# Kernel optimization log

Hardware: AMD Instinct MI355X
Metric: run time of the kernel (lower is better)

## Reference

```python
import jax, jax.numpy as jnp
import numpy as np

NUM_BINS = 15
GAMMA_INITIAL = 1.0
EPS = 1e-20


def setup_inputs() -> dict:
    key = jax.random.key(0)
    k1, k2 = jax.random.split(key)
    N, C = 1048576, 128
    inp = jax.random.normal(k1, (N, C), dtype=jnp.float32)
    target = jax.random.randint(k2, (N,), 0, C, dtype=jnp.int64)
    # bin_stats from __init__: bin i covers [i/num_bins, (i+1)/num_bins), gamma=gamma_initial
    bin_uppers = (jnp.arange(1, NUM_BINS, dtype=jnp.float32) / NUM_BINS)  # interior boundaries [num_bins-1]
    gammas = jnp.full((NUM_BINS,), GAMMA_INITIAL, dtype=jnp.float32)
    return {"input": inp, "target": target, "bin_uppers": bin_uppers, "gammas": gammas}


def reference(input, target, bin_uppers, gammas):
    # [N, C] logits -> per-sample logpt at target class
    logp = jax.nn.log_softmax(input, axis=1)                       # [N, C]
    logpt = jnp.take_along_axis(logp, target[:, None], axis=1)[:, 0]  # [N]
    pt = jnp.exp(logpt)                                            # [N]
    # vectorized replacement of the Python bin-search: pt in [lower, upper) -> bin index
    # (first bin catches pt < uppers[0], last bin catches pt >= uppers[-1])
    bin_idx = jnp.searchsorted(bin_uppers, pt, side="right")       # [N] in [0, num_bins-1]
    gamma = gammas[bin_idx]                                        # [N] (gamma lookup, detached in original)
    gamma_sign = jnp.sign(gamma)
    gamma_mag = jnp.abs(gamma)
    loss = -((1.0 - gamma_sign * pt + EPS) ** gamma_mag) * logpt
    return loss.sum()
```

## Files before the change

kernel.cpp:

```cpp
#include <hip/hip_runtime.h>

#define NBINS 15

typedef float f32x4 __attribute__((ext_vector_type(4)));

__device__ __forceinline__ float rdlane_f(float v, int lane) {
    return __int_as_float(__builtin_amdgcn_readlane(__float_as_int(v), lane));
}

template <int CTRL, int RMASK>
__device__ __forceinline__ float dpp_add(float e) {
    int moved = __builtin_amdgcn_update_dpp(0, __float_as_int(e), CTRL, RMASK, 0xf, true);
    return e + __int_as_float(moved);
}

__device__ __forceinline__ float half32_sum(float e) {
    e = dpp_add<0x111, 0xf>(e);
    e = dpp_add<0x112, 0xf>(e);
    e = dpp_add<0x114, 0xf>(e);
    e = dpp_add<0x118, 0xf>(e);
    e = dpp_add<0x142, 0xa>(e);
    return e;
}

__global__ __launch_bounds__(256) void adafocal_partial(
    const float* __restrict__ inp,
    const int* __restrict__ target,
    const float* __restrict__ bin_uppers,
    const float* __restrict__ gammas,
    float* __restrict__ partial,
    int N)
{
    __shared__ float  s_g[NBINS];
    __shared__ float2 s_coll[4][128];
    __shared__ float  s_wsum[4];

    if (threadIdx.x < NBINS) s_g[threadIdx.x] = gammas[threadIdx.x];
    __syncthreads();

    float u[NBINS - 1];
    #pragma unroll
    for (int i = 0; i < NBINS - 1; ++i) u[i] = bin_uppers[i];

    const int lane  = threadIdx.x & 63;
    const int wid   = threadIdx.x >> 6;
    const int gwave = blockIdx.x * 4 + wid;
    const int wrow0 = gwave * 128;

    int2 tt = make_int2(0, 0);
    if (wrow0 + 2 * lane + 1 < N)      tt = ((const int2*)target)[(wrow0 >> 1) + lane];
    else if (wrow0 + 2 * lane < N)     tt.x = target[wrow0 + 2 * lane];

    if (wrow0 + 128 <= N) {
        #pragma unroll 4
        for (int k = 0; k < 64; ++k) {
            const f32x4 v = __builtin_nontemporal_load(
                (const f32x4*)(inp + (size_t)(wrow0 + 2 * k) * 128) + lane);

            float e = __expf(v.x) + __expf(v.y) + __expf(v.z) + __expf(v.w);
            e = half32_sum(e);

            const int t0 = __builtin_amdgcn_readlane(tt.x, k);
            const int t1 = __builtin_amdgcn_readlane(tt.y, k);
            const float a0  = (t0 & 1) ? v.y : v.x;
            const float b0  = (t0 & 1) ? v.w : v.z;
            const float xt0 = rdlane_f((t0 & 2) ? b0 : a0, t0 >> 2);
            const float a1  = (t1 & 1) ? v.y : v.x;
            const float b1  = (t1 & 1) ? v.w : v.z;
            const float xt1 = rdlane_f((t1 & 2) ? b1 : a1, 32 + (t1 >> 2));

            float2 val;
            val.x = e;
            val.y = (lane < 32) ? xt0 : xt1;
            if ((lane & 31) == 31)
                s_coll[wid][2 * k + (lane >> 5)] = val;
        }
    } else {
        s_coll[wid][lane]      = make_float2(1.0f, 0.0f);
        s_coll[wid][64 + lane] = make_float2(1.0f, 0.0f);
        for (int k = 0; k < 64; ++k) {
            const int grow = wrow0 + 2 * k;
            if (grow >= N) break;
            const bool full = (grow + 1 < N);
            f32x4 v = {0.f, 0.f, 0.f, 0.f};
            if (full || lane < 32)
                v = *((const f32x4*)(inp + (size_t)grow * 128) + lane);
            float e = __expf(v.x) + __expf(v.y) + __expf(v.z) + __expf(v.w);
            e = half32_sum(e);
            const int t0 = __builtin_amdgcn_readlane(tt.x, k);
            const int t1 = __builtin_amdgcn_readlane(tt.y, k);
            const float a0  = (t0 & 1) ? v.y : v.x;
            const float b0  = (t0 & 1) ? v.w : v.z;
            const float xt0 = rdlane_f((t0 & 2) ? b0 : a0, t0 >> 2);
            const float a1  = (t1 & 1) ? v.y : v.x;
            const float b1  = (t1 & 1) ? v.w : v.z;
            const float xt1 = rdlane_f((t1 & 2) ? b1 : a1, 32 + (t1 >> 2));
            float2 val;
            val.x = e;
            val.y = (lane < 32) ? xt0 : xt1;
            if (lane == 31 || (full && lane == 63))
                s_coll[wid][2 * k + (lane >> 5)] = val;
        }
    }

    float acc = 0.0f;
    #pragma unroll
    for (int h = 0; h < 2; ++h) {
        const float2 cv   = s_coll[wid][64 * h + lane];
        const float logpt = cv.y - __logf(cv.x);
        const float pt    = __expf(logpt);

        int b = 0;
        #pragma unroll
        for (int i = 0; i < NBINS - 1; ++i)
            b += (u[i] <= pt) ? 1 : 0;

        const float g     = s_g[b];
        const float gsign = (g > 0.0f) ? 1.0f : (g < 0.0f ? -1.0f : 0.0f);
        const float gmag  = fabsf(g);
        const float base  = 1.0f - gsign * pt + 1e-20f;
        const float powv  = (gmag == 1.0f) ? base : __powf(base, gmag);
        acc -= powv * logpt;
    }

    #pragma unroll
    for (int m = 1; m < 64; m <<= 1)
        acc += __shfl_xor(acc, m);
    if (lane == 0) s_wsum[wid] = acc;
    __syncthreads();
    if (threadIdx.x == 0)
        partial[blockIdx.x] = (s_wsum[0] + s_wsum[1]) + (s_wsum[2] + s_wsum[3]);
}

__global__ __launch_bounds__(256) void adafocal_final(
    const float* __restrict__ partial, float* __restrict__ out, int nblocks)
{
    __shared__ float s_wsum[4];
    float acc = 0.0f;
    for (int i = threadIdx.x; i < nblocks; i += 256) acc += partial[i];
    #pragma unroll
    for (int m = 1; m < 64; m <<= 1)
        acc += __shfl_xor(acc, m);
    const int lane = threadIdx.x & 63;
    const int wid  = threadIdx.x >> 6;
    if (lane == 0) s_wsum[wid] = acc;
    __syncthreads();
    if (threadIdx.x == 0)
        out[0] = (s_wsum[0] + s_wsum[1]) + (s_wsum[2] + s_wsum[3]);
}

extern "C" void kernel_launch(void* const* d_in, const int* in_sizes, int n_in,
                              void* d_out, int out_size, void* d_ws, size_t ws_size,
                              hipStream_t stream) {
    const float* inp        = (const float*)d_in[0];
    const int*   targetp    = (const int*)d_in[1];
    const float* bin_uppers = (const float*)d_in[2];
    const float* gammas     = (const float*)d_in[3];
    float* out = (float*)d_out;

    const int N = in_sizes[1];
    const int nwaves  = (N + 127) / 128;
    const int nblocks = (nwaves + 3) / 4;

    float* partial = (float*)d_ws;

    adafocal_partial<<<nblocks, 256, 0, stream>>>(inp, targetp, bin_uppers, gammas, partial, N);
    adafocal_final<<<1, 256, 0, stream>>>(partial, out, nblocks);
}
```

Measured before the change: 95.48 us.

## Fuse final reduction into main kernel via last-block atomic counter

```diff
diff --git a/kernel.cpp b/kernel.cpp
--- a/kernel.cpp
+++ b/kernel.cpp
@@ -6,6 +6,9 @@
 
 __device__ __forceinline__ float rdlane_f(float v, int lane) {
     return __int_as_float(__builtin_amdgcn_readlane(__float_as_int(v), lane));
+}
+__device__ __forceinline__ float rdfirst_f(float v) {
+    return __int_as_float(__builtin_amdgcn_readfirstlane(__float_as_int(v)));
 }
 
 template <int CTRL, int RMASK>
@@ -23,24 +26,27 @@
     return e;
 }
 
-__global__ __launch_bounds__(256) void adafocal_partial(
+__global__ __launch_bounds__(256) void adafocal_fused(
     const float* __restrict__ inp,
     const int* __restrict__ target,
     const float* __restrict__ bin_uppers,
     const float* __restrict__ gammas,
+    float* __restrict__ out,
+    unsigned int* __restrict__ counter,
     float* __restrict__ partial,
     int N)
 {
     __shared__ float  s_g[NBINS];
     __shared__ float2 s_coll[4][128];
     __shared__ float  s_wsum[4];
+    __shared__ int    s_last;
 
     if (threadIdx.x < NBINS) s_g[threadIdx.x] = gammas[threadIdx.x];
     __syncthreads();
 
     float u[NBINS - 1];
     #pragma unroll
-    for (int i = 0; i < NBINS - 1; ++i) u[i] = bin_uppers[i];
+    for (int i = 0; i < NBINS - 1; ++i) u[i] = rdfirst_f(bin_uppers[i]);
 
     const int lane  = threadIdx.x & 63;
     const int wid   = threadIdx.x >> 6;
@@ -52,7 +58,7 @@
     else if (wrow0 + 2 * lane < N)     tt.x = target[wrow0 + 2 * lane];
 
     if (wrow0 + 128 <= N) {
-        #pragma unroll 4
+        #pragma unroll 8
         for (int k = 0; k < 64; ++k) {
             const f32x4 v = __builtin_nontemporal_load(
                 (const f32x4*)(inp + (size_t)(wrow0 + 2 * k) * 128) + lane);
@@ -128,25 +134,29 @@
         acc += __shfl_xor(acc, m);
     if (lane == 0) s_wsum[wid] = acc;
     __syncthreads();
-    if (threadIdx.x == 0)
+
+    if (threadIdx.x == 0) {
         partial[blockIdx.x] = (s_wsum[0] + s_wsum[1]) + (s_wsum[2] + s_wsum[3]);
-}
+        __threadfence();
+        unsigned int old = __hip_atomic_fetch_add(counter, 1u, __ATOMIC_ACQ_REL,
+                                                  __HIP_MEMORY_SCOPE_AGENT);
+        s_last = (old == gridDim.x - 1) ? 1 : 0;
+    }
+    __syncthreads();
 
-__global__ __launch_bounds__(256) void adafocal_final(
-    const float* __restrict__ partial, float* __restrict__ out, int nblocks)
-{
-    __shared__ float s_wsum[4];
-    float acc = 0.0f;
-    for (int i = threadIdx.x; i < nblocks; i += 256) acc += partial[i];
-    #pragma unroll
-    for (int m = 1; m < 64; m <<= 1)
-        acc += __shfl_xor(acc, m);
-    const int lane = threadIdx.x & 63;
-    const int wid  = threadIdx.x >> 6;
-    if (lane == 0) s_wsum[wid] = acc;
-    __syncthreads();
-    if (threadIdx.x == 0)
-        out[0] = (s_wsum[0] + s_wsum[1]) + (s_wsum[2] + s_wsum[3]);
+    if (s_last) {
+        float a2 = 0.0f;
+        for (unsigned int i = threadIdx.x; i < gridDim.x; i += 256)
+            a2 += __hip_atomic_load(&partial[i], __ATOMIC_RELAXED,
+                                    __HIP_MEMORY_SCOPE_AGENT);
+        #pragma unroll
+        for (int m = 1; m < 64; m <<= 1)
+            a2 += __shfl_xor(a2, m);
+        if (lane == 0) s_wsum[wid] = a2;
+        __syncthreads();
+        if (threadIdx.x == 0)
+            out[0] = (s_wsum[0] + s_wsum[1]) + (s_wsum[2] + s_wsum[3]);
+    }
 }
 
 extern "C" void kernel_launch(void* const* d_in, const int* in_sizes, int n_in,
@@ -162,8 +172,10 @@
     const int nwaves  = (N + 127) / 128;
     const int nblocks = (nwaves + 3) / 4;
 
-    float* partial = (float*)d_ws;
+    unsigned int* counter = (unsigned int*)d_ws;
+    float* partial = (float*)((char*)d_ws + 1024);
 
-    adafocal_partial<<<nblocks, 256, 0, stream>>>(inp, targetp, bin_uppers, gammas, partial, N);
-    adafocal_final<<<1, 256, 0, stream>>>(partial, out, nblocks);
+    hipMemsetAsync(counter, 0, sizeof(unsigned int), stream);
+    adafocal_fused<<<nblocks, 256, 0, stream>>>(inp, targetp, bin_uppers, gammas,
+                                                out, counter, partial, N);
 }
```

New measurement: 252.8 us. +164.7%, slower.
